# Kernel tuning notes

Measured on AMD Instinct MI355X. Metric: run time of the kernel, lower is better.

The kernel has to match this reference:

```python
import jax, jax.numpy as jnp
import numpy as np

B, IN_CAPS, IN_DIM = 256, 1152, 8
NUM_CAPS, DIM_VEC = 10, 16
NUM_ROUTING = 3


def squash(v, axis=-1):
    # scale = |v|^2 / (1+|v|^2) / |v|
    s2 = jnp.sum(jnp.square(v), axis=axis, keepdims=True)
    scale = s2 / (1.0 + s2) / jnp.sqrt(s2)
    return scale * v


def setup_inputs() -> dict:
    key = jax.random.key(0)
    k1, k2 = jax.random.split(key)
    inputs = jax.random.normal(k1, (B, IN_CAPS, IN_DIM), dtype=jnp.float32)
    W = jax.random.normal(k2, (IN_CAPS, NUM_CAPS, IN_DIM, DIM_VEC), dtype=jnp.float32) * 0.05
    bias = jnp.zeros((1, IN_CAPS, NUM_CAPS), dtype=jnp.float32)
    return {"inputs": inputs, "W": W, "bias": bias}


def reference(inputs, W, bias):
    # inputs_hat[b,i,j,d] = sum_e inputs[b,i,e] * W[i,j,e,d]
    hat = jnp.einsum('bie,ijed->bijd', inputs, W)  # [B, ic, nc, dv]
    b_logits = bias  # [1, ic, nc], broadcasts to [B, ic, nc] after first update
    outputs = None
    for r in range(NUM_ROUTING):
        c = jax.nn.softmax(b_logits, axis=2)            # coupling over output caps
        s = jnp.sum(c[..., None] * hat, axis=1)         # [B, nc, dv]
        outputs = squash(s)                             # [B, nc, dv]
        if r != NUM_ROUTING - 1:
            # agreement: <hat[b,i,j,:], v[b,j,:]>
            b_logits = b_logits + jnp.einsum('bijd,bjd->bij', hat, outputs)
    return outputs  # [B, num_capsule, dim_vector]
```

## Files before the change

### kernel.cpp

```cpp
#include <hip/hip_runtime.h>
#include <hip/hip_fp16.h>


#define IC 1152
#define IE 8
#define NC 10
#define DV 16
#define NB 256
#define NW (IC * NC * IE * DV)
#define SOUT (NC * DV)
#define NWAVE 12
#define TPB (NWAVE * 64)
#define NGPW 3

typedef _Float16 h2 __attribute__((ext_vector_type(2)));
union WChunk { int4 v; h2 p[4]; _Float16 h[8]; };
union XFrag { int4 v; h2 p[4]; };

#if defined(__has_builtin) && __has_builtin(__builtin_amdgcn_fdot2)
__device__ inline float fdot2(h2 a, h2 b, float c) {
    return __builtin_amdgcn_fdot2(a, b, c, false);
}
#else
__device__ inline float fdot2(h2 a, h2 b, float c) {
    return fmaf((float)a.x, (float)b.x, fmaf((float)a.y, (float)b.y, c));
}
#endif

__global__ void wprep_kernel(const float* __restrict__ W, int4* __restrict__ Wc) {
    const int t = blockIdx.x * blockDim.x + threadIdx.x;
    if (t >= NW / 8) return;
    const int lane = t & 63;
    const int h = lane >> 5, r = lane & 31;
    const int k = (t >> 6) & 7;
    const int r2 = t >> 9;
    const int j = r2 % NC, Gp = r2 / NC;
    const int i = Gp * 32 + r;
    const int d = h * 8 + k;
    const float* src = W + ((size_t)(i * NC + j) * IE) * DV + d;
    WChunk c;
#pragma unroll
    for (int e = 0; e < IE; ++e) c.h[e] = (_Float16)src[(size_t)e * DV];
    Wc[t] = c.v;
}

__device__ inline void butterfly_acc(const float* s8, int r, float* slab8) {
    float t4[4];
#pragma unroll
    for (int d = 0; d < 4; ++d) {
        const bool hi = (r & 16);
        const float mine = hi ? s8[d + 4] : s8[d];
        const float send = hi ? s8[d] : s8[d + 4];
        t4[d] = mine + __shfl_xor(send, 16);
    }
    float t2[2];
#pragma unroll
    for (int d = 0; d < 2; ++d) {
        const bool hi = (r & 8);
        const float mine = hi ? t4[d + 2] : t4[d];
        const float send = hi ? t4[d] : t4[d + 2];
        t2[d] = mine + __shfl_xor(send, 8);
    }
    float t1;
    {
        const bool hi = (r & 4);
        const float mine = hi ? t2[1] : t2[0];
        const float send = hi ? t2[0] : t2[1];
        t1 = mine + __shfl_xor(send, 4);
    }
    t1 += __shfl_xor(t1, 2);
    t1 += __shfl_xor(t1, 1);
    if ((r & 3) == 0) {
        const int dl = (r >> 2) & 7;
        slab8[dl] += t1;
    }
}

template <int RD>
__global__ __launch_bounds__(TPB) void round_caps(
    const float* __restrict__ X,
    const int4* __restrict__ Wc,
    const float* __restrict__ bias,
    const float* __restrict__ v_in,
    float* __restrict__ v_out)
{
    __shared__ float s_part[NWAVE * SOUT];
    __shared__ __align__(16) h2 v2s[SOUT / 2];

    const int b = blockIdx.x;
    const int tid = threadIdx.x;
    const int w = tid >> 6;
    const int g = tid & 63;
    const int h = g >> 5;
    const int r = g & 31;

    float vkeep = 0.f;
    if constexpr (RD > 0) {
        if (RD == 1 && tid < SOUT) vkeep = v_in[(size_t)b * SOUT + tid];
        if (tid < SOUT / 2) {
            const float* vp = v_in + (size_t)b * SOUT + 2 * tid;
            v2s[tid] = h2{(_Float16)vp[0], (_Float16)vp[1]};
        }
    }
    for (int idx = g; idx < SOUT; idx += 64) s_part[w * SOUT + idx] = 0.f;
    if constexpr (RD > 0) __syncthreads();

#pragma unroll
    for (int gl = 0; gl < NGPW; ++gl) {
        const int Gp = NGPW * w + gl;
        const int i = Gp * 32 + r;

        XFrag xu;
        {
            const float4* xr = (const float4*)(X + ((size_t)b * IC + i) * IE);
            const float4 x0 = xr[0], x1 = xr[1];
            xu.p[0] = h2{(_Float16)x0.x, (_Float16)x0.y};
            xu.p[1] = h2{(_Float16)x0.z, (_Float16)x0.w};
            xu.p[2] = h2{(_Float16)x1.x, (_Float16)x1.y};
            xu.p[3] = h2{(_Float16)x1.z, (_Float16)x1.w};
        }
        const int4* wpg = Wc + (size_t)(Gp * NC) * 512 + g;
        float* slab = &s_part[w * SOUT + h * 8];

        if constexpr (RD == 0) {
            float cj[NC];
            float Z = 0.f;
#pragma unroll
            for (int j = 0; j < NC; ++j) {
                const float e = __expf(bias[i * NC + j]);
                cj[j] = e;
                Z += e;
            }
            const float rz = 1.f / Z;
#pragma unroll
            for (int j = 0; j < NC; ++j) cj[j] *= rz;

#pragma unroll
            for (int j = 0; j < NC; ++j) {
                const int4* wp = wpg + j * 512;
                float s8[8];
#pragma unroll
                for (int kp = 0; kp < 4; ++kp) {
                    WChunk w0, w1;
                    w0.v = wp[(2 * kp) * 64];
                    w1.v = wp[(2 * kp + 1) * 64];
                    float a0 = 0.f, a1 = 0.f;
#pragma unroll
                    for (int q = 0; q < 4; ++q) {
                        a0 = fdot2(xu.p[q], w0.p[q], a0);
                        a1 = fdot2(xu.p[q], w1.p[q], a1);
                    }
                    s8[2 * kp] = cj[j] * a0;
                    s8[2 * kp + 1] = cj[j] * a1;
                }
                butterfly_acc(s8, r, slab + j * DV);
            }
        } else {
            h2 hat2[NC][4];
            float cj[NC];
            float Z = 0.f;
#pragma unroll
            for (int j = 0; j < NC; ++j) {
                const int4* wp = wpg + j * 512;
#pragma unroll
                for (int kp = 0; kp < 4; ++kp) {
                    WChunk w0, w1;
                    w0.v = wp[(2 * kp) * 64];
                    w1.v = wp[(2 * kp + 1) * 64];
                    float a0 = 0.f, a1 = 0.f;
#pragma unroll
                    for (int q = 0; q < 4; ++q) {
                        a0 = fdot2(xu.p[q], w0.p[q], a0);
                        a1 = fdot2(xu.p[q], w1.p[q], a1);
                    }
                    hat2[j][kp] = h2{(_Float16)a0, (_Float16)a1};
                }
                XFrag vv;
                vv.v = *(const int4*)(v2s + (j * 8 + h * 4));
                float ah = 0.f;
#pragma unroll
                for (int q = 0; q < 4; ++q) ah = fdot2(hat2[j][q], vv.p[q], ah);
                const float lt = bias[i * NC + j] + ah + __shfl_xor(ah, 32);
                const float e = __expf(lt);
                cj[j] = e;
                Z += e;
            }
            const float rz = 1.f / Z;

#pragma unroll
            for (int j = 0; j < NC; ++j) {
                const float cn = cj[j] * rz;
                float s8[8];
#pragma unroll
                for (int q = 0; q < 4; ++q) {
                    s8[2 * q]     = cn * (float)hat2[j][q].x;
                    s8[2 * q + 1] = cn * (float)hat2[j][q].y;
                }
                butterfly_acc(s8, r, slab + j * DV);
            }
        }
    }
    __syncthreads();

    if (tid < SOUT) {
        float sv = 0.f;
#pragma unroll
        for (int ww = 0; ww < NWAVE; ++ww) sv += s_part[ww * SOUT + tid];
        float s2 = sv * sv;
#pragma unroll
        for (int mk = 8; mk >= 1; mk >>= 1) s2 += __shfl_xor(s2, mk, 16);
        const float scale = sqrtf(s2) / (1.f + s2);
        float vv = scale * sv;
        if constexpr (RD == 1) vv += vkeep;
        v_out[(size_t)b * SOUT + tid] = vv;
    }
}

extern "C" void kernel_launch(void* const* d_in, const int* in_sizes, int n_in,
                              void* d_out, int out_size, void* d_ws, size_t ws_size,
                              hipStream_t stream) {
    const float* X = (const float*)d_in[0];
    const float* W = (const float*)d_in[1];
    const float* bias = (const float*)d_in[2];
    float* out = (float*)d_out;

    int4* Wc = (int4*)d_ws;
    float* v1 = (float*)(Wc + NW / 8);
    float* vsum = v1 + (size_t)NB * SOUT;

    wprep_kernel<<<dim3(720), dim3(256), 0, stream>>>(W, Wc);

    dim3 grid(NB);
    round_caps<0><<<grid, TPB, 0, stream>>>(X, Wc, bias, nullptr, v1);
    round_caps<1><<<grid, TPB, 0, stream>>>(X, Wc, bias, v1, vsum);
    round_caps<2><<<grid, TPB, 0, stream>>>(X, Wc, bias, vsum, out);
}
```

Before: 176.6 us.

## Split input capsules across two blocks per batch, deferring squash to consumers

Each batch item is now handled by two blocks, each covering half of the input-capsule groups (9 waves x 2 groups instead of 12 x 3). The blocks write partial sums, and the next round (or a new final kernel) adds the two halves and applies the squash. Bias is padded to 12 floats per row so it can be read as vector loads. The launch count doubles, which raises parallelism on a 256-CU part, at the cost of an extra kernel launch, partial-sum traffic, and squash work repeated by both halves.

```diff
diff --git a/kernel.cpp b/kernel.cpp
--- a/kernel.cpp
+++ b/kernel.cpp
@@ -9,9 +9,10 @@
 #define NB 256
 #define NW (IC * NC * IE * DV)
 #define SOUT (NC * DV)
-#define NWAVE 12
+#define NWAVE 9
 #define TPB (NWAVE * 64)
-#define NGPW 3
+#define NGPW 2
+#define HGP 18
 
 typedef _Float16 h2 __attribute__((ext_vector_type(2)));
 union WChunk { int4 v; h2 p[4]; _Float16 h[8]; };
@@ -44,6 +45,12 @@
     Wc[t] = c.v;
 }
 
+__global__ void bprep_kernel(const float* __restrict__ bias, float* __restrict__ biasP) {
+    const int t = blockIdx.x * blockDim.x + threadIdx.x;
+    const int i = t / 12, j = t - i * 12;
+    biasP[t] = (j < NC) ? bias[i * NC + j] : 0.f;
+}
+
 __device__ inline void butterfly_acc(const float* s8, int r, float* slab8) {
     float t4[4];
 #pragma unroll
@@ -80,26 +87,37 @@
 __global__ __launch_bounds__(TPB) void round_caps(
     const float* __restrict__ X,
     const int4* __restrict__ Wc,
-    const float* __restrict__ bias,
-    const float* __restrict__ v_in,
-    float* __restrict__ v_out)
+    const float* __restrict__ biasP,
+    const float* __restrict__ spIn,
+    float* __restrict__ v1g,
+    float* __restrict__ spOut)
 {
     __shared__ float s_part[NWAVE * SOUT];
     __shared__ __align__(16) h2 v2s[SOUT / 2];
 
-    const int b = blockIdx.x;
+    const int half = blockIdx.x;
+    const int b = blockIdx.y;
     const int tid = threadIdx.x;
     const int w = tid >> 6;
     const int g = tid & 63;
     const int h = g >> 5;
     const int r = g & 31;
 
-    float vkeep = 0.f;
     if constexpr (RD > 0) {
-        if (RD == 1 && tid < SOUT) vkeep = v_in[(size_t)b * SOUT + tid];
-        if (tid < SOUT / 2) {
-            const float* vp = v_in + (size_t)b * SOUT + 2 * tid;
-            v2s[tid] = h2{(_Float16)vp[0], (_Float16)vp[1]};
+        if (tid < SOUT) {
+            float sv = spIn[(size_t)b * SOUT + tid] +
+                       spIn[((size_t)NB + b) * SOUT + tid];
+            float s2 = sv * sv;
+#pragma unroll
+            for (int mk = 8; mk >= 1; mk >>= 1) s2 += __shfl_xor(s2, mk, 16);
+            float vv = sqrtf(s2) / (1.f + s2) * sv;
+            if constexpr (RD == 2) {
+                vv += v1g[(size_t)b * SOUT + tid];
+            } else {
+                if (half == 0) v1g[(size_t)b * SOUT + tid] = vv;
+            }
+            const float oth = __shfl_xor(vv, 1);
+            if (!(tid & 1)) v2s[tid >> 1] = h2{(_Float16)vv, (_Float16)oth};
         }
     }
     for (int idx = g; idx < SOUT; idx += 64) s_part[w * SOUT + idx] = 0.f;
@@ -107,7 +125,7 @@
 
 #pragma unroll
     for (int gl = 0; gl < NGPW; ++gl) {
-        const int Gp = NGPW * w + gl;
+        const int Gp = half * HGP + NGPW * w + gl;
         const int i = Gp * 32 + r;
 
         XFrag xu;
@@ -119,6 +137,14 @@
             xu.p[2] = h2{(_Float16)x1.x, (_Float16)x1.y};
             xu.p[3] = h2{(_Float16)x1.z, (_Float16)x1.w};
         }
+        float bl[12];
+        {
+            const float4* bp4 = (const float4*)(biasP + (size_t)i * 12);
+            const float4 b0 = bp4[0], b1 = bp4[1], b2 = bp4[2];
+            bl[0] = b0.x; bl[1] = b0.y; bl[2] = b0.z; bl[3] = b0.w;
+            bl[4] = b1.x; bl[5] = b1.y; bl[6] = b1.z; bl[7] = b1.w;
+            bl[8] = b2.x; bl[9] = b2.y; bl[10] = b2.z; bl[11] = b2.w;
+        }
         const int4* wpg = Wc + (size_t)(Gp * NC) * 512 + g;
         float* slab = &s_part[w * SOUT + h * 8];
 
@@ -127,7 +153,7 @@
             float Z = 0.f;
 #pragma unroll
             for (int j = 0; j < NC; ++j) {
-                const float e = __expf(bias[i * NC + j]);
+                const float e = __expf(bl[j]);
                 cj[j] = e;
                 Z += e;
             }
@@ -180,7 +206,7 @@
                 float ah = 0.f;
 #pragma unroll
                 for (int q = 0; q < 4; ++q) ah = fdot2(hat2[j][q], vv.p[q], ah);
-                const float lt = bias[i * NC + j] + ah + __shfl_xor(ah, 32);
+                const float lt = bl[j] + ah + __shfl_xor(ah, 32);
                 const float e = __expf(lt);
                 cj[j] = e;
                 Z += e;
@@ -206,13 +232,19 @@
         float sv = 0.f;
 #pragma unroll
         for (int ww = 0; ww < NWAVE; ++ww) sv += s_part[ww * SOUT + tid];
+        spOut[((size_t)half * NB + b) * SOUT + tid] = sv;
+    }
+}
+
+__global__ __launch_bounds__(192) void final_squash(const float* __restrict__ sp,
+                                                    float* __restrict__ out) {
+    const int b = blockIdx.x, t = threadIdx.x;
+    if (t < SOUT) {
+        float sv = sp[(size_t)b * SOUT + t] + sp[((size_t)NB + b) * SOUT + t];
         float s2 = sv * sv;
 #pragma unroll
         for (int mk = 8; mk >= 1; mk >>= 1) s2 += __shfl_xor(s2, mk, 16);
-        const float scale = sqrtf(s2) / (1.f + s2);
-        float vv = scale * sv;
-        if constexpr (RD == 1) vv += vkeep;
-        v_out[(size_t)b * SOUT + tid] = vv;
+        out[(size_t)b * SOUT + t] = sqrtf(s2) / (1.f + s2) * sv;
     }
 }
 
@@ -225,13 +257,18 @@
     float* out = (float*)d_out;
 
     int4* Wc = (int4*)d_ws;
-    float* v1 = (float*)(Wc + NW / 8);
-    float* vsum = v1 + (size_t)NB * SOUT;
+    float* biasP = (float*)(Wc + NW / 8);
+    float* v1g = biasP + IC * 12;
+    float* spA = v1g + (size_t)NB * SOUT;
+    float* spB = spA + 2ull * NB * SOUT;
+    float* spC = spB + 2ull * NB * SOUT;
 
     wprep_kernel<<<dim3(720), dim3(256), 0, stream>>>(W, Wc);
-
-    dim3 grid(NB);
-    round_caps<0><<<grid, TPB, 0, stream>>>(X, Wc, bias, nullptr, v1);
-    round_caps<1><<<grid, TPB, 0, stream>>>(X, Wc, bias, v1, vsum);
-    round_caps<2><<<grid, TPB, 0, stream>>>(X, Wc, bias, vsum, out);
-}
+    bprep_kernel<<<dim3(54), dim3(256), 0, stream>>>(bias, biasP);
+
+    dim3 grid(2, NB);
+    round_caps<0><<<grid, TPB, 0, stream>>>(X, Wc, biasP, nullptr, nullptr, spA);
+    round_caps<1><<<grid, TPB, 0, stream>>>(X, Wc, biasP, spA, v1g, spB);
+    round_caps<2><<<grid, TPB, 0, stream>>>(X, Wc, biasP, spB, v1g, spC);
+    final_squash<<<dim3(NB), dim3(192), 0, stream>>>(spC, out);
+}
```

Result: no change. 178.8 us (+1.2%).

## Split routing by capsule group with LDS-staged weights and separate reduction kernels

Applied to the files above, without the earlier changes.

Changes the grid from one block per batch item to a 2D grid over input-capsule groups and batch tiles. Each block stages one group's fp16 weights in shared memory and reuses them across 8 batch items, one per wave. Per-group partial sums go to global memory, and a separate reduce kernel sums them, applies squash and writes the fp16 output vector for the next round. The aim is to cut repeated global weight reads per batch item, at the cost of extra kernel launches and the partial-sum traffic.

```diff
diff --git a/kernel.cpp b/kernel.cpp
--- a/kernel.cpp
+++ b/kernel.cpp
@@ -9,9 +9,10 @@
 #define NB 256
 #define NW (IC * NC * IE * DV)
 #define SOUT (NC * DV)
-#define NWAVE 12
-#define TPB (NWAVE * 64)
-#define NGPW 3
+#define GPB (IC / 32)
+#define NBB 8
+#define TPB (NBB * 64)
+#define WSLOT (NC * 8 * 64)
 
 typedef _Float16 h2 __attribute__((ext_vector_type(2)));
 union WChunk { int4 v; h2 p[4]; _Float16 h[8]; };
@@ -44,7 +45,7 @@
     Wc[t] = c.v;
 }
 
-__device__ inline void butterfly_acc(const float* s8, int r, float* slab8) {
+__device__ inline void butterfly_store(const float* s8, int r, float* dst8) {
     float t4[4];
 #pragma unroll
     for (int d = 0; d < 4; ++d) {
@@ -72,7 +73,7 @@
     t1 += __shfl_xor(t1, 1);
     if ((r & 3) == 0) {
         const int dl = (r >> 2) & 7;
-        slab8[dl] += t1;
+        dst8[dl] = t1;
     }
 }
 
@@ -81,138 +82,148 @@
     const float* __restrict__ X,
     const int4* __restrict__ Wc,
     const float* __restrict__ bias,
-    const float* __restrict__ v_in,
-    float* __restrict__ v_out)
+    const h2* __restrict__ vredH,
+    float* __restrict__ sp)
 {
-    __shared__ float s_part[NWAVE * SOUT];
-    __shared__ __align__(16) h2 v2s[SOUT / 2];
-
-    const int b = blockIdx.x;
+    __shared__ __align__(16) int4 Ws[WSLOT];
+
+    const int Gp = blockIdx.x;
+    const int bg = blockIdx.y;
     const int tid = threadIdx.x;
     const int w = tid >> 6;
     const int g = tid & 63;
     const int h = g >> 5;
     const int r = g & 31;
 
-    float vkeep = 0.f;
-    if constexpr (RD > 0) {
-        if (RD == 1 && tid < SOUT) vkeep = v_in[(size_t)b * SOUT + tid];
-        if (tid < SOUT / 2) {
-            const float* vp = v_in + (size_t)b * SOUT + 2 * tid;
-            v2s[tid] = h2{(_Float16)vp[0], (_Float16)vp[1]};
-        }
-    }
-    for (int idx = g; idx < SOUT; idx += 64) s_part[w * SOUT + idx] = 0.f;
-    if constexpr (RD > 0) __syncthreads();
-
-#pragma unroll
-    for (int gl = 0; gl < NGPW; ++gl) {
-        const int Gp = NGPW * w + gl;
-        const int i = Gp * 32 + r;
-
-        XFrag xu;
-        {
-            const float4* xr = (const float4*)(X + ((size_t)b * IC + i) * IE);
-            const float4 x0 = xr[0], x1 = xr[1];
-            xu.p[0] = h2{(_Float16)x0.x, (_Float16)x0.y};
-            xu.p[1] = h2{(_Float16)x0.z, (_Float16)x0.w};
-            xu.p[2] = h2{(_Float16)x1.x, (_Float16)x1.y};
-            xu.p[3] = h2{(_Float16)x1.z, (_Float16)x1.w};
-        }
-        const int4* wpg = Wc + (size_t)(Gp * NC) * 512 + g;
-        float* slab = &s_part[w * SOUT + h * 8];
-
-        if constexpr (RD == 0) {
-            float cj[NC];
-            float Z = 0.f;
-#pragma unroll
-            for (int j = 0; j < NC; ++j) {
-                const float e = __expf(bias[i * NC + j]);
-                cj[j] = e;
-                Z += e;
+    {
+        const int4* src = Wc + (size_t)Gp * WSLOT;
+#pragma unroll
+        for (int k = 0; k < WSLOT / TPB; ++k)
+            Ws[tid + k * TPB] = src[tid + k * TPB];
+    }
+
+    const int b = bg * NBB + w;
+    const int i = Gp * 32 + r;
+
+    XFrag xu;
+    {
+        const float4* xr = (const float4*)(X + ((size_t)b * IC + i) * IE);
+        const float4 x0 = xr[0], x1 = xr[1];
+        xu.p[0] = h2{(_Float16)x0.x, (_Float16)x0.y};
+        xu.p[1] = h2{(_Float16)x0.z, (_Float16)x0.w};
+        xu.p[2] = h2{(_Float16)x1.x, (_Float16)x1.y};
+        xu.p[3] = h2{(_Float16)x1.z, (_Float16)x1.w};
+    }
+
+    float cj[NC];
+    float Z = 0.f;
+    if constexpr (RD == 0) {
+#pragma unroll
+        for (int j = 0; j < NC; ++j) {
+            const float e = __expf(bias[i * NC + j]);
+            cj[j] = e;
+            Z += e;
+        }
+        const float rz = 1.f / Z;
+#pragma unroll
+        for (int j = 0; j < NC; ++j) cj[j] *= rz;
+    }
+
+    __syncthreads();
+
+    float* spb = sp + ((size_t)Gp * NB + b) * SOUT;
+
+    if constexpr (RD == 0) {
+#pragma unroll
+        for (int j = 0; j < NC; ++j) {
+            const int4* wp = Ws + j * 512 + g;
+            float s8[8];
+#pragma unroll
+            for (int kp = 0; kp < 4; ++kp) {
+                WChunk w0, w1;
+                w0.v = wp[(2 * kp) * 64];
+                w1.v = wp[(2 * kp + 1) * 64];
+                float a0 = 0.f, a1 = 0.f;
+#pragma unroll
+                for (int q = 0; q < 4; ++q) {
+                    a0 = fdot2(xu.p[q], w0.p[q], a0);
+                    a1 = fdot2(xu.p[q], w1.p[q], a1);
+                }
+                s8[2 * kp] = cj[j] * a0;
+                s8[2 * kp + 1] = cj[j] * a1;
             }
-            const float rz = 1.f / Z;
-#pragma unroll
-            for (int j = 0; j < NC; ++j) cj[j] *= rz;
-
-#pragma unroll
-            for (int j = 0; j < NC; ++j) {
-                const int4* wp = wpg + j * 512;
-                float s8[8];
-#pragma unroll
-                for (int kp = 0; kp < 4; ++kp) {
-                    WChunk w0, w1;
-                    w0.v = wp[(2 * kp) * 64];
-                    w1.v = wp[(2 * kp + 1) * 64];
-                    float a0 = 0.f, a1 = 0.f;
-#pragma unroll
-                    for (int q = 0; q < 4; ++q) {
-                        a0 = fdot2(xu.p[q], w0.p[q], a0);
-                        a1 = fdot2(xu.p[q], w1.p[q], a1);
-                    }
-                    s8[2 * kp] = cj[j] * a0;
-                    s8[2 * kp + 1] = cj[j] * a1;
+            butterfly_store(s8, r, spb + j * DV + h * 8);
+        }
+    } else {
+        h2 hat2[NC][4];
+#pragma unroll
+        for (int j = 0; j < NC; ++j) {
+            const int4* wp = Ws + j * 512 + g;
+#pragma unroll
+            for (int kp = 0; kp < 4; ++kp) {
+                WChunk w0, w1;
+                w0.v = wp[(2 * kp) * 64];
+                w1.v = wp[(2 * kp + 1) * 64];
+                float a0 = 0.f, a1 = 0.f;
+#pragma unroll
+                for (int q = 0; q < 4; ++q) {
+                    a0 = fdot2(xu.p[q], w0.p[q], a0);
+                    a1 = fdot2(xu.p[q], w1.p[q], a1);
                 }
-                butterfly_acc(s8, r, slab + j * DV);
+                hat2[j][kp] = h2{(_Float16)a0, (_Float16)a1};
             }
-        } else {
-            h2 hat2[NC][4];
-            float cj[NC];
-            float Z = 0.f;
-#pragma unroll
-            for (int j = 0; j < NC; ++j) {
-                const int4* wp = wpg + j * 512;
-#pragma unroll
-                for (int kp = 0; kp < 4; ++kp) {
-                    WChunk w0, w1;
-                    w0.v = wp[(2 * kp) * 64];
-                    w1.v = wp[(2 * kp + 1) * 64];
-                    float a0 = 0.f, a1 = 0.f;
-#pragma unroll
-                    for (int q = 0; q < 4; ++q) {
-                        a0 = fdot2(xu.p[q], w0.p[q], a0);
-                        a1 = fdot2(xu.p[q], w1.p[q], a1);
-                    }
-                    hat2[j][kp] = h2{(_Float16)a0, (_Float16)a1};
-                }
-                XFrag vv;
-                vv.v = *(const int4*)(v2s + (j * 8 + h * 4));
-                float ah = 0.f;
-#pragma unroll
-                for (int q = 0; q < 4; ++q) ah = fdot2(hat2[j][q], vv.p[q], ah);
-                const float lt = bias[i * NC + j] + ah + __shfl_xor(ah, 32);
-                const float e = __expf(lt);
-                cj[j] = e;
-                Z += e;
+            XFrag vv;
+            vv.v = *(const int4*)(vredH + (size_t)b * (SOUT / 2) + j * 8 + h * 4);
+            float ah = 0.f;
+#pragma unroll
+            for (int q = 0; q < 4; ++q) ah = fdot2(hat2[j][q], vv.p[q], ah);
+            const float lt = bias[i * NC + j] + ah + __shfl_xor(ah, 32);
+            const float e = __expf(lt);
+            cj[j] = e;
+            Z += e;
+        }
+        const float rz = 1.f / Z;
+
+#pragma unroll
+        for (int j = 0; j < NC; ++j) {
+            const float cn = cj[j] * rz;
+            float s8[8];
+#pragma unroll
+            for (int q = 0; q < 4; ++q) {
+                s8[2 * q]     = cn * (float)hat2[j][q].x;
+                s8[2 * q + 1] = cn * (float)hat2[j][q].y;
             }
-            const float rz = 1.f / Z;
-
-#pragma unroll
-            for (int j = 0; j < NC; ++j) {
-                const float cn = cj[j] * rz;
-                float s8[8];
-#pragma unroll
-                for (int q = 0; q < 4; ++q) {
-                    s8[2 * q]     = cn * (float)hat2[j][q].x;
-                    s8[2 * q + 1] = cn * (float)hat2[j][q].y;
-                }
-                butterfly_acc(s8, r, slab + j * DV);
-            }
-        }
-    }
-    __syncthreads();
-
-    if (tid < SOUT) {
-        float sv = 0.f;
-#pragma unroll
-        for (int ww = 0; ww < NWAVE; ++ww) sv += s_part[ww * SOUT + tid];
-        float s2 = sv * sv;
-#pragma unroll
-        for (int mk = 8; mk >= 1; mk >>= 1) s2 += __shfl_xor(s2, mk, 16);
-        const float scale = sqrtf(s2) / (1.f + s2);
-        float vv = scale * sv;
-        if constexpr (RD == 1) vv += vkeep;
-        v_out[(size_t)b * SOUT + tid] = vv;
+            butterfly_store(s8, r, spb + j * DV + h * 8);
+        }
+    }
+}
+
+template <int P>
+__global__ __launch_bounds__(192) void reduce_caps(
+    const float* __restrict__ sp,
+    const float* __restrict__ vprevF,
+    float* __restrict__ voutF,
+    h2* __restrict__ voutH,
+    float* __restrict__ out)
+{
+    const int b = blockIdx.x, t = threadIdx.x;
+    if (t >= SOUT) return;
+    float sv = 0.f;
+#pragma unroll
+    for (int gq = 0; gq < GPB; ++gq) sv += sp[((size_t)gq * NB + b) * SOUT + t];
+    float s2 = sv * sv;
+#pragma unroll
+    for (int mk = 8; mk >= 1; mk >>= 1) s2 += __shfl_xor(s2, mk, 16);
+    float vv = sqrtf(s2) / (1.f + s2) * sv;
+    if constexpr (P == 2) vv += vprevF[(size_t)b * SOUT + t];
+    if constexpr (P == 3) {
+        out[(size_t)b * SOUT + t] = vv;
+        return;
+    } else {
+        if constexpr (P == 1) voutF[(size_t)b * SOUT + t] = vv;
+        const float oth = __shfl_xor(vv, 1);
+        if (!(t & 1))
+            voutH[(size_t)b * (SOUT / 2) + (t >> 1)] = h2{(_Float16)vv, (_Float16)oth};
     }
 }
 
@@ -225,13 +236,20 @@
     float* out = (float*)d_out;
 
     int4* Wc = (int4*)d_ws;
-    float* v1 = (float*)(Wc + NW / 8);
-    float* vsum = v1 + (size_t)NB * SOUT;
+    float* spA = (float*)(Wc + NW / 8);
+    float* spB = spA + (size_t)GPB * NB * SOUT;
+    float* spC = spB + (size_t)GPB * NB * SOUT;
+    float* v1F = spC + (size_t)GPB * NB * SOUT;
+    h2* vH1 = (h2*)(v1F + (size_t)NB * SOUT);
+    h2* vH2 = vH1 + (size_t)NB * (SOUT / 2);
 
     wprep_kernel<<<dim3(720), dim3(256), 0, stream>>>(W, Wc);
 
-    dim3 grid(NB);
-    round_caps<0><<<grid, TPB, 0, stream>>>(X, Wc, bias, nullptr, v1);
-    round_caps<1><<<grid, TPB, 0, stream>>>(X, Wc, bias, v1, vsum);
-    round_caps<2><<<grid, TPB, 0, stream>>>(X, Wc, bias, vsum, out);
-}
+    dim3 rg(GPB, NB / NBB);
+    round_caps<0><<<rg, TPB, 0, stream>>>(X, Wc, bias, nullptr, spA);
+    reduce_caps<1><<<dim3(NB), dim3(192), 0, stream>>>(spA, nullptr, v1F, vH1, nullptr);
+    round_caps<1><<<rg, TPB, 0, stream>>>(X, Wc, bias, vH1, spB);
+    reduce_caps<2><<<dim3(NB), dim3(192), 0, stream>>>(spB, v1F, nullptr, vH2, nullptr);
+    round_caps<2><<<rg, TPB, 0, stream>>>(X, Wc, bias, vH2, spC);
+    reduce_caps<3><<<dim3(NB), dim3(192), 0, stream>>>(spC, nullptr, nullptr, nullptr, out);
+}
```

Result: faster. 152.9 us (-13.5%).
